# Kernel optimization log

Hardware: AMD Instinct MI355X
Metric: run time of the kernel (lower is better)

The kernel has to match this reference:

```python
import jax, jax.numpy as jnp
import numpy as np

U, V = 208, 176  # hard-coded DFT output shape from the original DFT2D
B, C, KH, KW = 32, 8, 3, 3


def dft2d(p):
    """Faithful vectorization of the original nested-loop DFT2D.
    dft[l, k] = (1/(M*N)) * sum_{m,n} p[m,n] * exp(-2j*pi*(k*m/V + l*n/U)),
    output shape (U, V) = (208, 176). Note the (intentionally) non-standard
    normalization axes, copied exactly from the source.
    """
    M, N = p.shape
    km = jnp.outer(jnp.arange(V), jnp.arange(M)).astype(jnp.float32)  # (V, M)
    ln = jnp.outer(jnp.arange(U), jnp.arange(N)).astype(jnp.float32)  # (U, N)
    E1 = jnp.exp(-2j * jnp.pi * km / V)  # (V, M) complex64
    E2 = jnp.exp(-2j * jnp.pi * ln / U)  # (U, N) complex64
    return jnp.einsum('km,mn,ln->lk', E1, p.astype(jnp.complex64), E2) / (M * N)


def setup_inputs() -> dict:
    key = jax.random.key(0)
    k1, k2 = jax.random.split(key)
    x = jax.random.normal(k1, (B, C, U, V), dtype=jnp.float32)
    kernel = jax.random.normal(k2, (KH, KW, 1, 1), dtype=jnp.float32)
    bias = jnp.zeros((1,), dtype=jnp.float32)
    return {"x": x, "kernel": kernel, "bias": bias}


def reference(x, kernel, bias):
    # Build the symmetric spatial kernel: [[k, flip_h(k)], [flip_w(k), flip_hw(k)]]
    k2 = kernel[::-1, :, :, :]
    k3 = kernel[:, ::-1, :, :]
    k4 = kernel[::-1, ::-1, :, :]
    sk = jnp.concatenate([jnp.concatenate([kernel, k2], axis=0),
                          jnp.concatenate([k3, k4], axis=0)], axis=1)  # (2KH, 2KW, 1, 1)
    sk2d = sk[:, :, 0, 0]  # tf.squeeze -> (2KH, 2KW)

    # k-space representation of the kernel and 50th-percentile binary mask
    fft_k = dft2d(sk2d)  # (208, 176) complex
    r = jnp.real(fft_k)
    thr = jnp.percentile(r, 50.0, method='nearest')  # tfp.stats.percentile default
    mask = (r > thr).astype(jnp.float32)  # (208, 176)

    # FFT of the image over its innermost two dims, mask in k-space, inverse FFT
    fft_x = jnp.fft.fft2(x)  # (B, C, 208, 176) complex64
    out = jnp.abs(jnp.fft.ifft2(fft_x * mask))  # bias unused on the test path
    return out
```

## Files before the change

kernel.cpp:

```cpp
#include <hip/hip_runtime.h>
#include <math.h>

#define UU 208
#define VV 176
#define NPIX (UU*VV)
#define MASKBLKS 143
#define ROWBLKS 1664

typedef __attribute__((ext_vector_type(2))) float v2f;
typedef __attribute__((ext_vector_type(4))) float v4f;

__device__ __forceinline__ v2f mk2(float x, float y){ v2f r; r.x = x; r.y = y; return r; }
__device__ __forceinline__ v2f sp(float s){ v2f r; r.x = s; r.y = s; return r; }

template<bool INV>
__device__ __forceinline__ v2f cmulc(v2f a, float wx, float wy_fwd){
  const float wy = INV ? -wy_fwd : wy_fwd;
  return sp(a.x) * mk2(wx, wy) + sp(a.y) * mk2(-wy, wx);
}
__device__ __forceinline__ v2f cmulw4(v2f a, v4f t){
  return sp(a.x) * mk2(t.x, t.y) + sp(a.y) * mk2(t.z, t.w);
}
__device__ __forceinline__ v2f cmulw4i(v2f a, v4f t){
  return sp(a.x) * mk2(t.x, t.z) + sp(a.y) * mk2(t.y, t.w);
}

template<bool INV>
__device__ __forceinline__ void dft4(v2f& x0, v2f& x1, v2f& x2, v2f& x3){
  v2f s0 = x0 + x2, d0 = x0 - x2;
  v2f s1 = x1 + x3, d1 = x1 - x3;
  v2f jd1;
  if (INV){ jd1.x = -d1.y; jd1.y =  d1.x; }
  else    { jd1.x =  d1.y; jd1.y = -d1.x; }
  x0 = s0 + s1; x2 = s0 - s1;
  x1 = d0 + jd1; x3 = d0 - jd1;
}

template<bool INV>
__device__ __forceinline__ void fft16(v2f v[16]){
  dft4<INV>(v[0], v[4], v[8],  v[12]);
  dft4<INV>(v[1], v[5], v[9],  v[13]);
  dft4<INV>(v[2], v[6], v[10], v[14]);
  dft4<INV>(v[3], v[7], v[11], v[15]);
  const float C1 = 0.92387953251128674f;
  const float S1 = 0.38268343236508978f;
  const float R2 = 0.70710678118654752f;
  v[5]  = cmulc<INV>(v[5],  C1, -S1);
  v[9]  = cmulc<INV>(v[9],  R2, -R2);
  v[13] = cmulc<INV>(v[13], S1, -C1);
  v[6]  = cmulc<INV>(v[6],  R2, -R2);
  v[10] = cmulc<INV>(v[10], 0.f, -1.f);
  v[14] = cmulc<INV>(v[14], -R2, -R2);
  v[7]  = cmulc<INV>(v[7],  S1, -C1);
  v[11] = cmulc<INV>(v[11], -R2, -R2);
  v[15] = cmulc<INV>(v[15], -C1,  S1);
  dft4<INV>(v[0],  v[1],  v[2],  v[3]);
  dft4<INV>(v[4],  v[5],  v[6],  v[7]);
  dft4<INV>(v[8],  v[9],  v[10], v[11]);
  dft4<INV>(v[12], v[13], v[14], v[15]);
}

template<int N, bool INV>
__device__ __forceinline__ void dftN(const v2f* __restrict__ t, v2f* __restrict__ F,
                                     const v2f* __restrict__ cs){
  const int H = N/2;
  v2f u[H], w[H];
  #pragma unroll
  for (int n = 1; n <= H; n++){ u[n-1] = t[n] + t[N-n]; w[n-1] = t[n] - t[N-n]; }
  v2f a = t[0];
  #pragma unroll
  for (int n = 0; n < H; n++) a += u[n];
  F[0] = a;
  #pragma unroll
  for (int k = 1; k <= H; k++){
    v2f C = t[0], S = sp(0.f);
    #pragma unroll
    for (int n = 1; n <= H; n++){
      const int idx = (n * k) % N;
      C += u[n-1] * sp(cs[idx].x);
      S += w[n-1] * sp(cs[idx].y);
    }
    v2f ssw; ssw.x = S.y; ssw.y = -S.x;
    if (!INV){ F[k] = C + ssw; F[N-k] = C - ssw; }
    else     { F[k] = C - ssw; F[N-k] = C + ssw; }
  }
}

__device__ __forceinline__ unsigned sortable(float f){
  unsigned u = __float_as_uint(f);
  return (u & 0x80000000u) ? ~u : (u | 0x80000000u);
}

__device__ __forceinline__ unsigned find_bucket(const unsigned* __restrict__ bins_g,
                                                unsigned* sWS, unsigned* sB, unsigned* sK){
  const int t = threadIdx.x, lane = t & 63, wv = t >> 6;
  unsigned c = bins_g[t];
  unsigned v = c;
  #pragma unroll
  for (int d = 1; d < 64; d <<= 1){
    unsigned u = __shfl_up(v, d, 64);
    if (lane >= d) v += u;
  }
  if (lane == 63) sWS[wv] = v;
  __syncthreads();
  unsigned woff = 0;
  #pragma unroll
  for (int j = 0; j < 3; j++) woff += (j < wv) ? sWS[j] : 0u;
  unsigned incl = v + woff, excl = incl - c;
  unsigned k = *sK;
  __syncthreads();
  if (k >= excl && k < incl){ *sB = (unsigned)t; *sK = k - excl; }
  __syncthreads();
  return *sB;
}

__global__ __launch_bounds__(256) void rowfft_mask(const float* __restrict__ x, v2f* __restrict__ freq,
                                                   const float* __restrict__ kin, float* __restrict__ rbuf,
                                                   unsigned* __restrict__ bins24){
  const double PI2 = 6.283185307179586476925286766559;
  __shared__ v4f wf[VV];
  __shared__ v2f cs11[11];
  __shared__ v2f mid[16][177];
  if (blockIdx.x >= ROWBLKS){
    unsigned* h = (unsigned*)mid;
    h[threadIdx.x] = 0u;
    int i = (blockIdx.x - ROWBLKS) * 256 + threadIdx.x;
    int l = i / VV, k = i - l * VV;
    double c1, s1, c2, s2;
    { double a = PI2 * (double)k / (double)VV; c1 = cos(a); s1 = sin(a); }
    { double a = PI2 * (double)l / (double)UU; c2 = cos(a); s2 = sin(a); }
    double cA[6], sA[6], cB[6], sB[6];
    cA[0] = 1.0; sA[0] = 0.0; cA[1] = c1; sA[1] = s1;
    cB[0] = 1.0; sB[0] = 0.0; cB[1] = c2; sB[1] = s2;
    #pragma unroll
    for (int m = 2; m < 6; m++){
      cA[m] = 2.0*c1*cA[m-1] - cA[m-2];
      sA[m] = 2.0*c1*sA[m-1] - sA[m-2];
      cB[m] = 2.0*c2*cB[m-1] - cB[m-2];
      sB[m] = 2.0*c2*sB[m-1] - sB[m-2];
    }
    const int rm[6] = {0, 1, 2, 2, 1, 0};
    double P[3], Q[3];
    #pragma unroll
    for (int a = 0; a < 3; a++){
      P[a] = 0.0; Q[a] = 0.0;
      #pragma unroll
      for (int n = 0; n < 6; n++){
        double kv = (double)kin[a*3 + rm[n]];
        P[a] += kv * cB[n];
        Q[a] += kv * sB[n];
      }
    }
    double s = 0.0;
    #pragma unroll
    for (int m = 0; m < 6; m++)
      s += cA[m]*P[rm[m]] - sA[m]*Q[rm[m]];
    float val = (float)(s / 36.0);
    rbuf[i] = val;
    __syncthreads();
    atomicAdd(&h[sortable(val) >> 24], 1u);
    __syncthreads();
    if (h[threadIdx.x]) atomicAdd(&bins24[threadIdx.x], h[threadIdx.x]);
    return;
  }
  { int i = threadIdx.x;
    if (i < VV){
      double a = -PI2 * (double)i / (double)VV;
      float c = (float)cos(a), s = (float)sin(a);
      v4f f; f.x = c; f.y = s; f.z = -s; f.w = c; wf[i] = f;
    }
    if (i < 11){
      double a = PI2 * (double)i / 11.0;
      cs11[i] = mk2((float)cos(a), (float)sin(a));
    } }
  const int gr = threadIdx.x >> 4, ln = threadIdx.x & 15;
  const int row = blockIdx.x * 16 + gr;
  const int p = row / UU, rr = row - p * UU;
  const float* xr1 = x + ((size_t)(2*p) * UU + rr) * VV;
  const float* xr2 = xr1 + (size_t)NPIX;
  v2f* fr = freq + (size_t)row * VV;
  __syncthreads();
  if (ln < 11){
    v2f v[16];
    #pragma unroll
    for (int a = 0; a < 16; a++) v[a] = mk2(xr1[11*a + ln], xr2[11*a + ln]);
    fft16<false>(v);
    #pragma unroll
    for (int j = 0; j < 16; j++)
      mid[gr][j*11 + ln] = cmulw4(v[4*(j&3) + (j>>2)], wf[ln*j]);
  }
  v2f t[11], F[11];
  #pragma unroll
  for (int n2 = 0; n2 < 11; n2++) t[n2] = mid[gr][ln*11 + n2];
  dftN<11,false>(t, F, cs11);
  #pragma unroll
  for (int k2 = 0; k2 < 11; k2++) fr[ln + 16*k2] = F[k2];
}

template<int LEVEL>
__global__ __launch_bounds__(256) void hist_pass(const float* __restrict__ rbuf,
                                                 const unsigned* __restrict__ binsAll,
                                                 unsigned* __restrict__ binsOut){
  __shared__ unsigned h[256];
  __shared__ unsigned sWS[4];
  __shared__ unsigned sB, sK;
  if (threadIdx.x == 0) sK = 18304u;
  h[threadIdx.x] = 0u;
  __syncthreads();
  unsigned prefix = find_bucket(binsAll, sWS, &sB, &sK) << 24;
  if (LEVEL >= 2) prefix |= find_bucket(binsAll + 256, sWS, &sB, &sK) << 16;
  if (LEVEL >= 3) prefix |= find_bucket(binsAll + 512, sWS, &sB, &sK) << 8;
  const int SHIFT = 24 - 8*LEVEL;
  int i = blockIdx.x * 256 + threadIdx.x;
  unsigned u = sortable(rbuf[i]);
  if ((u >> (SHIFT + 8)) == (prefix >> (SHIFT + 8)))
    atomicAdd(&h[(u >> SHIFT) & 255u], 1u);
  __syncthreads();
  if (h[threadIdx.x]) atomicAdd(&binsOut[threadIdx.x], h[threadIdx.x]);
}

__global__ __launch_bounds__(256) void thr_final(const unsigned* __restrict__ binsAll,
                                                 float* __restrict__ thrOut){
  __shared__ unsigned sWS[4];
  __shared__ unsigned sB, sK;
  if (threadIdx.x == 0) sK = 18304u;
  __syncthreads();
  unsigned prefix = find_bucket(binsAll,       sWS, &sB, &sK) << 24;
  prefix |= find_bucket(binsAll + 256, sWS, &sB, &sK) << 16;
  prefix |= find_bucket(binsAll + 512, sWS, &sB, &sK) << 8;
  prefix |= find_bucket(binsAll + 768, sWS, &sB, &sK);
  if (threadIdx.x == 0){
    unsigned u = prefix;
    u = (u & 0x80000000u) ? (u ^ 0x80000000u) : ~u;
    thrOut[0] = __uint_as_float(u);
  }
}

__global__ __launch_bounds__(256) void colfft(v2f* __restrict__ freq,
                                              const float* __restrict__ rbuf, const float* __restrict__ thrp){
  __shared__ v4f wf[UU];
  __shared__ v2f cs13[13];
  __shared__ v2f buf[UU*17];
  { int i = threadIdx.x;
    const double PI2 = 6.283185307179586476925286766559;
    if (i < UU){
      double a = -PI2 * (double)i / (double)UU;
      float c = (float)cos(a), s = (float)sin(a);
      v4f f; f.x = c; f.y = s; f.z = -s; f.w = c; wf[i] = f;
    }
    if (i < 13){
      double a = PI2 * (double)i / 13.0;
      cs13[i] = mk2((float)cos(a), (float)sin(a));
    } }
  const int role = threadIdx.x >> 4, c = threadIdx.x & 15;
  const int img = blockIdx.x / 11;
  const int v0 = (blockIdx.x - img*11) << 4;
  v2f* base = freq + (size_t)img * NPIX + v0 + c;
  const float thr = thrp[0];
  __syncthreads();
  if (role < 13){
    v2f v[16];
    #pragma unroll
    for (int a = 0; a < 16; a++) v[a] = base[(13*a + role)*VV];
    fft16<false>(v);
    #pragma unroll
    for (int j = 0; j < 16; j++)
      buf[(j*13 + role)*17 + c] = cmulw4(v[4*(j&3) + (j>>2)], wf[role*j]);
  }
  __syncthreads();
  v2f F[13];
  {
    v2f t[13];
    #pragma unroll
    for (int n2 = 0; n2 < 13; n2++) t[n2] = buf[(role*13 + n2)*17 + c];
    dftN<13,false>(t, F, cs13);
    #pragma unroll
    for (int k2 = 0; k2 < 13; k2++){
      int u = role + 16*k2;
      float m = (rbuf[u*VV + v0 + c] > thr) ? 1.0f : 0.0f;
      F[k2] *= sp(m);
    }
  }
  __syncthreads();
  #pragma unroll
  for (int k2 = 0; k2 < 13; k2++) buf[(role + 16*k2)*17 + c] = F[k2];
  __syncthreads();
  if (role < 13){
    v2f v[16];
    #pragma unroll
    for (int a = 0; a < 16; a++) v[a] = buf[(13*a + role)*17 + c];
    fft16<true>(v);
    #pragma unroll
    for (int j = 0; j < 16; j++)
      buf[(j*13 + role)*17 + c] = cmulw4i(v[4*(j&3) + (j>>2)], wf[role*j]);
  }
  __syncthreads();
  {
    v2f t[13], G[13];
    #pragma unroll
    for (int n2 = 0; n2 < 13; n2++) t[n2] = buf[(role*13 + n2)*17 + c];
    dftN<13,true>(t, G, cs13);
    #pragma unroll
    for (int k2 = 0; k2 < 13; k2++)
      base[(role + 16*k2)*VV] = G[k2];
  }
}

__global__ __launch_bounds__(256) void rowifft_abs(const v2f* __restrict__ freq, float* __restrict__ out){
  __shared__ v4f wf[VV];
  __shared__ v2f cs11[11];
  __shared__ v2f mid[16][177];
  { int i = threadIdx.x;
    const double PI2 = 6.283185307179586476925286766559;
    if (i < VV){
      double a = -PI2 * (double)i / (double)VV;
      float c = (float)cos(a), s = (float)sin(a);
      v4f f; f.x = c; f.y = s; f.z = -s; f.w = c; wf[i] = f;
    }
    if (i < 11){
      double a = PI2 * (double)i / 11.0;
      cs11[i] = mk2((float)cos(a), (float)sin(a));
    } }
  const int gr = threadIdx.x >> 4, ln = threadIdx.x & 15;
  const int row = blockIdx.x * 16 + gr;
  const int p = row / UU, rr = row - p * UU;
  const v2f* fr = freq + (size_t)row * VV;
  float* orow1 = out + ((size_t)(2*p) * UU + rr) * VV;
  float* orow2 = orow1 + (size_t)NPIX;
  __syncthreads();
  if (ln < 11){
    v2f v[16];
    #pragma unroll
    for (int a = 0; a < 16; a++) v[a] = fr[11*a + ln];
    fft16<true>(v);
    #pragma unroll
    for (int j = 0; j < 16; j++)
      mid[gr][j*11 + ln] = cmulw4i(v[4*(j&3) + (j>>2)], wf[ln*j]);
  }
  v2f t[11], G[11];
  #pragma unroll
  for (int n2 = 0; n2 < 11; n2++) t[n2] = mid[gr][ln*11 + n2];
  dftN<11,true>(t, G, cs11);
  #pragma unroll
  for (int k2 = 0; k2 < 11; k2++){
    orow1[ln + 16*k2] = fabsf(G[k2].x) * (1.0f / 36608.0f);
    orow2[ln + 16*k2] = fabsf(G[k2].y) * (1.0f / 36608.0f);
  }
}

extern "C" void kernel_launch(void* const* d_in, const int* in_sizes, int n_in,
                              void* d_out, int out_size, void* d_ws, size_t ws_size,
                              hipStream_t stream){
  const float* x   = (const float*)d_in[0];
  const float* kin = (const float*)d_in[1];
  float* out = (float*)d_out;
  char* ws = (char*)d_ws;
  v2f*      freq = (v2f*)ws;
  float*    rbuf = (float*)(ws + 37486592);
  float*    thr  = (float*)(ws + 37633024);
  unsigned* bins = (unsigned*)(ws + 37633040);

  hipMemsetAsync(bins, 0, 4*256*4, stream);
  hipLaunchKernelGGL(rowfft_mask,  dim3(ROWBLKS + MASKBLKS), dim3(256), 0, stream, x, freq, kin, rbuf, bins);
  hipLaunchKernelGGL(hist_pass<1>, dim3(143),  dim3(256), 0, stream, rbuf, bins, bins + 256);
  hipLaunchKernelGGL(hist_pass<2>, dim3(143),  dim3(256), 0, stream, rbuf, bins, bins + 512);
  hipLaunchKernelGGL(hist_pass<3>, dim3(143),  dim3(256), 0, stream, rbuf, bins, bins + 768);
  hipLaunchKernelGGL(thr_final,    dim3(1),    dim3(256), 0, stream, bins, thr);
  hipLaunchKernelGGL(colfft,       dim3(1408), dim3(256), 0, stream, freq, rbuf, thr);
  hipLaunchKernelGGL(rowifft_abs,  dim3(1664), dim3(256), 0, stream, freq, out);
}
```

Measured before the change: 69.34 us.

## Replace four-level radix select with 16-bit histogram plus shortlist threshold pick

The median-threshold search now uses one 65536-bin global histogram of the top 16 bits, built directly with global atomics in the mask blocks. A shortlist kernel finds the target bucket and compacts the matching values, and a single-block kernel resolves the low 16 bits from that shortlist. This cuts the launch chain from four histogram/threshold kernels to two, removing several launch gaps and repeated full passes over the mask values. In exchange it adds a larger memset, contended global atomics, and a shortlist kernel in which every block rescans the 256KB histogram.

```diff
diff --git a/kernel.cpp b/kernel.cpp
--- a/kernel.cpp
+++ b/kernel.cpp
@@ -91,10 +91,8 @@
   return (u & 0x80000000u) ? ~u : (u | 0x80000000u);
 }
 
-__device__ __forceinline__ unsigned find_bucket(const unsigned* __restrict__ bins_g,
-                                                unsigned* sWS, unsigned* sB, unsigned* sK){
-  const int t = threadIdx.x, lane = t & 63, wv = t >> 6;
-  unsigned c = bins_g[t];
+__device__ __forceinline__ void blockscan(unsigned c, unsigned* sWS, unsigned& excl, unsigned& incl){
+  const int lane = threadIdx.x & 63, wv = threadIdx.x >> 6;
   unsigned v = c;
   #pragma unroll
   for (int d = 1; d < 64; d <<= 1){
@@ -106,24 +104,54 @@
   unsigned woff = 0;
   #pragma unroll
   for (int j = 0; j < 3; j++) woff += (j < wv) ? sWS[j] : 0u;
-  unsigned incl = v + woff, excl = incl - c;
-  unsigned k = *sK;
-  __syncthreads();
-  if (k >= excl && k < incl){ *sB = (unsigned)t; *sK = k - excl; }
-  __syncthreads();
-  return *sB;
+  incl = v + woff; excl = incl - c;
+}
+
+__device__ __forceinline__ unsigned find256(const unsigned* bins, unsigned* sWS,
+                                            unsigned* sRes, unsigned* kRef){
+  unsigned c = bins[threadIdx.x];
+  unsigned excl, incl;
+  blockscan(c, sWS, excl, incl);
+  unsigned k = *kRef;
+  if (k >= excl && k < incl){ sRes[0] = (unsigned)threadIdx.x; sRes[1] = k - excl; }
+  __syncthreads();
+  unsigned b = sRes[0]; *kRef = sRes[1];
+  __syncthreads();
+  return b;
+}
+
+__device__ __forceinline__ unsigned find64k(const unsigned* __restrict__ bins,
+                                            unsigned* sWS, unsigned* sRes, unsigned* kRef){
+  const int t = threadIdx.x;
+  const uint4* b4 = (const uint4*)bins + t*64;
+  unsigned s = 0;
+  #pragma unroll 16
+  for (int j = 0; j < 64; j++){ uint4 q = b4[j]; s += q.x + q.y + q.z + q.w; }
+  unsigned excl, incl;
+  blockscan(s, sWS, excl, incl);
+  unsigned k = *kRef;
+  if (k >= excl && k < incl){ sRes[0] = (unsigned)t; sRes[1] = k - excl; }
+  __syncthreads();
+  unsigned t0 = sRes[0], kk = sRes[1];
+  __syncthreads();
+  unsigned c = bins[t0*256 + t];
+  blockscan(c, sWS, excl, incl);
+  if (kk >= excl && kk < incl){ sRes[0] = (unsigned)t; sRes[1] = kk - excl; }
+  __syncthreads();
+  unsigned b = t0*256 + sRes[0];
+  *kRef = sRes[1];
+  __syncthreads();
+  return b;
 }
 
 __global__ __launch_bounds__(256) void rowfft_mask(const float* __restrict__ x, v2f* __restrict__ freq,
                                                    const float* __restrict__ kin, float* __restrict__ rbuf,
-                                                   unsigned* __restrict__ bins24){
+                                                   unsigned* __restrict__ bins){
   const double PI2 = 6.283185307179586476925286766559;
   __shared__ v4f wf[VV];
   __shared__ v2f cs11[11];
   __shared__ v2f mid[16][177];
   if (blockIdx.x >= ROWBLKS){
-    unsigned* h = (unsigned*)mid;
-    h[threadIdx.x] = 0u;
     int i = (blockIdx.x - ROWBLKS) * 256 + threadIdx.x;
     int l = i / VV, k = i - l * VV;
     double c1, s1, c2, s2;
@@ -157,10 +185,7 @@
       s += cA[m]*P[rm[m]] - sA[m]*Q[rm[m]];
     float val = (float)(s / 36.0);
     rbuf[i] = val;
-    __syncthreads();
-    atomicAdd(&h[sortable(val) >> 24], 1u);
-    __syncthreads();
-    if (h[threadIdx.x]) atomicAdd(&bins24[threadIdx.x], h[threadIdx.x]);
+    atomicAdd(&bins[sortable(val) >> 16], 1u);
     return;
   }
   { int i = threadIdx.x;
@@ -197,40 +222,50 @@
   for (int k2 = 0; k2 < 11; k2++) fr[ln + 16*k2] = F[k2];
 }
 
-template<int LEVEL>
-__global__ __launch_bounds__(256) void hist_pass(const float* __restrict__ rbuf,
-                                                 const unsigned* __restrict__ binsAll,
-                                                 unsigned* __restrict__ binsOut){
+__global__ __launch_bounds__(256) void shortlist(const float* __restrict__ rbuf,
+                                                 const unsigned* __restrict__ bins,
+                                                 float* __restrict__ slist,
+                                                 unsigned* __restrict__ counter,
+                                                 unsigned* __restrict__ meta){
+  __shared__ unsigned sWS[4], sRes[2];
+  unsigned kk = 18304u;
+  unsigned b0 = find64k(bins, sWS, sRes, &kk);
+  if (blockIdx.x == 0 && threadIdx.x == 0){ meta[0] = b0; meta[1] = kk; }
+  int i = blockIdx.x * 256 + threadIdx.x;
+  float v = rbuf[i];
+  if ((sortable(v) >> 16) == b0){
+    unsigned idx = atomicAdd(counter, 1u);
+    slist[idx] = v;
+  }
+}
+
+__global__ __launch_bounds__(256) void thr_pick(const float* __restrict__ slist,
+                                                const unsigned* __restrict__ counter,
+                                                const unsigned* __restrict__ meta,
+                                                float* __restrict__ thrOut){
   __shared__ unsigned h[256];
-  __shared__ unsigned sWS[4];
-  __shared__ unsigned sB, sK;
-  if (threadIdx.x == 0) sK = 18304u;
-  h[threadIdx.x] = 0u;
-  __syncthreads();
-  unsigned prefix = find_bucket(binsAll, sWS, &sB, &sK) << 24;
-  if (LEVEL >= 2) prefix |= find_bucket(binsAll + 256, sWS, &sB, &sK) << 16;
-  if (LEVEL >= 3) prefix |= find_bucket(binsAll + 512, sWS, &sB, &sK) << 8;
-  const int SHIFT = 24 - 8*LEVEL;
-  int i = blockIdx.x * 256 + threadIdx.x;
-  unsigned u = sortable(rbuf[i]);
-  if ((u >> (SHIFT + 8)) == (prefix >> (SHIFT + 8)))
-    atomicAdd(&h[(u >> SHIFT) & 255u], 1u);
-  __syncthreads();
-  if (h[threadIdx.x]) atomicAdd(&binsOut[threadIdx.x], h[threadIdx.x]);
-}
-
-__global__ __launch_bounds__(256) void thr_final(const unsigned* __restrict__ binsAll,
-                                                 float* __restrict__ thrOut){
-  __shared__ unsigned sWS[4];
-  __shared__ unsigned sB, sK;
-  if (threadIdx.x == 0) sK = 18304u;
-  __syncthreads();
-  unsigned prefix = find_bucket(binsAll,       sWS, &sB, &sK) << 24;
-  prefix |= find_bucket(binsAll + 256, sWS, &sB, &sK) << 16;
-  prefix |= find_bucket(binsAll + 512, sWS, &sB, &sK) << 8;
-  prefix |= find_bucket(binsAll + 768, sWS, &sB, &sK);
-  if (threadIdx.x == 0){
-    unsigned u = prefix;
+  __shared__ unsigned sWS[4], sRes[2];
+  const int tid = threadIdx.x;
+  const unsigned n = counter[0];
+  unsigned kk = meta[1];
+  h[tid] = 0u;
+  __syncthreads();
+  for (unsigned i = tid; i < n; i += 256){
+    unsigned u = sortable(slist[i]);
+    atomicAdd(&h[(u >> 8) & 255u], 1u);
+  }
+  __syncthreads();
+  unsigned b1 = find256(h, sWS, sRes, &kk);
+  h[tid] = 0u;
+  __syncthreads();
+  for (unsigned i = tid; i < n; i += 256){
+    unsigned u = sortable(slist[i]);
+    if (((u >> 8) & 255u) == b1) atomicAdd(&h[u & 255u], 1u);
+  }
+  __syncthreads();
+  unsigned b2 = find256(h, sWS, sRes, &kk);
+  if (tid == 0){
+    unsigned u = (meta[0] << 16) | (b1 << 8) | b2;
     u = (u & 0x80000000u) ? (u ^ 0x80000000u) : ~u;
     thrOut[0] = __uint_as_float(u);
   }
@@ -355,17 +390,19 @@
   const float* kin = (const float*)d_in[1];
   float* out = (float*)d_out;
   char* ws = (char*)d_ws;
-  v2f*      freq = (v2f*)ws;
-  float*    rbuf = (float*)(ws + 37486592);
-  float*    thr  = (float*)(ws + 37633024);
-  unsigned* bins = (unsigned*)(ws + 37633040);
-
-  hipMemsetAsync(bins, 0, 4*256*4, stream);
-  hipLaunchKernelGGL(rowfft_mask,  dim3(ROWBLKS + MASKBLKS), dim3(256), 0, stream, x, freq, kin, rbuf, bins);
-  hipLaunchKernelGGL(hist_pass<1>, dim3(143),  dim3(256), 0, stream, rbuf, bins, bins + 256);
-  hipLaunchKernelGGL(hist_pass<2>, dim3(143),  dim3(256), 0, stream, rbuf, bins, bins + 512);
-  hipLaunchKernelGGL(hist_pass<3>, dim3(143),  dim3(256), 0, stream, rbuf, bins, bins + 768);
-  hipLaunchKernelGGL(thr_final,    dim3(1),    dim3(256), 0, stream, bins, thr);
-  hipLaunchKernelGGL(colfft,       dim3(1408), dim3(256), 0, stream, freq, rbuf, thr);
-  hipLaunchKernelGGL(rowifft_abs,  dim3(1664), dim3(256), 0, stream, freq, out);
-}
+  v2f*      freq    = (v2f*)ws;
+  float*    rbuf    = (float*)(ws + 37486592);
+  float*    thr     = (float*)(ws + 37633024);
+  unsigned* bins    = (unsigned*)(ws + 37633040);
+  unsigned* counter = (unsigned*)(ws + 37895184);
+  unsigned* meta    = (unsigned*)(ws + 37895188);
+  float*    slist   = (float*)(ws + 37895200);
+
+  hipMemsetAsync(bins, 0, 262144 + 16, stream);
+  hipLaunchKernelGGL(rowfft_mask, dim3(ROWBLKS + MASKBLKS), dim3(256), 0, stream,
+                     x, freq, kin, rbuf, bins);
+  hipLaunchKernelGGL(shortlist,   dim3(143),  dim3(256), 0, stream, rbuf, bins, slist, counter, meta);
+  hipLaunchKernelGGL(thr_pick,    dim3(1),    dim3(256), 0, stream, slist, counter, meta, thr);
+  hipLaunchKernelGGL(colfft,      dim3(1408), dim3(256), 0, stream, freq, rbuf, thr);
+  hipLaunchKernelGGL(rowifft_abs, dim3(1664), dim3(256), 0, stream, freq, out);
+}
```

Result: slower. 74.84 us (+7.9%).
